# Optimization experiments

Hardware: AMD Instinct MI355X
Metric: run time of the kernel (lower is better)

## Reference

```python
import jax, jax.numpy as jnp
import numpy as np

B, S, E, H = 2, 2048, 1024, 16
D = E // H  # head dim = 64

def setup_inputs() -> dict:
    key = jax.random.key(0)
    ks = jax.random.split(key, 7)
    mk = lambda k, shape, scale=1.0: (jax.random.normal(k, shape, dtype=jnp.float32) * scale)
    return {
        "query": mk(ks[0], (B, S, E)),
        "key": mk(ks[1], (B, S, E)),
        "value": mk(ks[2], (B, S, E)),
        "Wq": mk(ks[3], (E, E), 1.0 / np.sqrt(E)),
        "Wk": mk(ks[4], (E, E), 1.0 / np.sqrt(E)),
        "Wv": mk(ks[5], (E, E), 1.0 / np.sqrt(E)),
        "Wo": mk(ks[6], (E, E), 1.0 / np.sqrt(E)),
    }

def reference(query, key, value, Wq, Wk, Wv, Wo):
    # nn.Linear(bias=False): y = x @ W.T
    def split_heads(x):
        return x.reshape(B, -1, H, D).transpose(0, 2, 1, 3)  # [B,H,S,D]
    q = split_heads(query @ Wq.T)
    k = split_heads(key @ Wk.T)
    v = split_heads(value @ Wv.T)
    scores = jnp.einsum("bhqd,bhkd->bhqk", q, k) / jnp.sqrt(jnp.float32(D))
    attn = jax.nn.softmax(scores, axis=-1)  # dropout p=0 -> identity
    out = jnp.einsum("bhqk,bhkd->bhqd", attn, v)
    out = out.transpose(0, 2, 1, 3).reshape(B, -1, E)
    out = out @ Wo.T
    return out
```

## Files before the change

### kernel.cpp

```cpp
#include <hip/hip_runtime.h>
#include <stdint.h>

#define S_LEN 2048
#define HDIM  64
#define EMB   1024
#define NTOK  4096

typedef short bf16x8 __attribute__((ext_vector_type(8)));
typedef float f32x4  __attribute__((ext_vector_type(4)));
typedef uint32_t u32x4 __attribute__((ext_vector_type(4)));
typedef uint32_t u32x2 __attribute__((ext_vector_type(2)));

__device__ __forceinline__ unsigned short f32_bf16(float f) {
  union { float f; uint32_t u; } v; v.f = f;
  return (unsigned short)((v.u + 0x7fffu + ((v.u >> 16) & 1u)) >> 16);
}

__device__ __forceinline__ uint32_t fbits(float f) {
  union { float f; uint32_t u; } v; v.f = f; return v.u;
}

__device__ __forceinline__ uint32_t pack_bf16_trunc(float lo, float hi) {
  return __builtin_amdgcn_perm(fbits(hi), fbits(lo), 0x07060302u);
}

__device__ __forceinline__ uint32_t pack_bf16_rne(float lo, float hi) {
  return (uint32_t)f32_bf16(lo) | ((uint32_t)f32_bf16(hi) << 16);
}

__device__ __forceinline__ void async_ld16(const unsigned short* g, unsigned short* l) {
  __builtin_amdgcn_global_load_lds(
      (__attribute__((address_space(1))) unsigned int*)(uintptr_t)g,
      (__attribute__((address_space(3))) unsigned int*)l, 16, 0, 0);
}

__device__ __forceinline__ void p_swap(uint32_t& x, uint32_t& y) {
  u32x2 r1 = __builtin_amdgcn_permlane32_swap(x, y, false, false);
  uint32_t a = r1[0], b = r1[1];
#if __has_builtin(__builtin_amdgcn_permlane16_swap)
  u32x2 r2 = __builtin_amdgcn_permlane16_swap(a, b, false, false);
  x = r2[0]; y = r2[1];
#else
  asm volatile("v_permlane16_swap_b32 %0, %1" : "+v"(a), "+v"(b));
  x = a; y = b;
#endif
}

__device__ __forceinline__ void block_sync_lgkm() {
  asm volatile("s_waitcnt lgkmcnt(0)" ::: "memory");
  __builtin_amdgcn_s_barrier();
}

#define CL2 0.18033688f

__global__ void cast_all(const float* __restrict__ q, const float* __restrict__ k,
                         const float* __restrict__ v, const float* __restrict__ Wq,
                         const float* __restrict__ Wk, const float* __restrict__ Wv,
                         const float* __restrict__ Wo,
                         unsigned short* __restrict__ qb, unsigned short* __restrict__ kb,
                         unsigned short* __restrict__ vb, unsigned short* __restrict__ wqb,
                         unsigned short* __restrict__ wkb, unsigned short* __restrict__ wvb,
                         unsigned short* __restrict__ wob) {
  const int b = blockIdx.x;
  const float* src; unsigned short* dst; int base;
  float scl = 1.0f;
  if (b < 12288) {
    const int which = b >> 12; base = b & 4095;
    src = which == 0 ? q : which == 1 ? k : v;
    dst = which == 0 ? qb : which == 1 ? kb : vb;
  } else {
    const int bb = b - 12288, which = bb >> 10; base = bb & 1023;
    src = which == 0 ? Wq : which == 1 ? Wk : which == 2 ? Wv : Wo;
    dst = which == 0 ? wqb : which == 1 ? wkb : which == 2 ? wvb : wob;
    if (which == 0) scl = CL2;
  }
  const int i = base * 256 + threadIdx.x;
  float4 f = ((const float4*)src)[i];
  ushort4 o;
  o.x = f32_bf16(f.x * scl); o.y = f32_bf16(f.y * scl);
  o.z = f32_bf16(f.z * scl); o.w = f32_bf16(f.w * scl);
  ((ushort4*)dst)[i] = o;
}

__global__ __launch_bounds__(256)
void gemm_qkv(const unsigned short* __restrict__ qb, const unsigned short* __restrict__ kb,
              const unsigned short* __restrict__ vb, const unsigned short* __restrict__ wqb,
              const unsigned short* __restrict__ wkb, const unsigned short* __restrict__ wvb,
              unsigned short* __restrict__ Qh, unsigned short* __restrict__ Kh,
              unsigned short* __restrict__ Vt) {
  __shared__ __align__(16) unsigned short As[2 * 128 * 32];
  __shared__ __align__(16) unsigned short Bs[2 * 128 * 32];

  const int z  = blockIdx.z;
  const int bx = blockIdx.y;
  const int by = blockIdx.x;
  const unsigned short* Xp = z == 0 ? qb  : z == 1 ? kb  : vb;
  const unsigned short* Wp = z == 0 ? wqb : z == 1 ? wkb : wvb;

  const unsigned short *A, *B;
  int tileM, tileN;
  if (z < 2) { A = Wp; tileM = bx * 128; B = Xp; tileN = by * 128; }
  else       { A = Xp; tileM = by * 128; B = Wp; tileN = bx * 128; }

  const int tid  = threadIdx.x;
  const int lane = tid & 63;
  const int wave = tid >> 6;
  const int wm = (wave >> 1) * 64;
  const int wn = (wave & 1) * 64;
  const int ccol = lane & 15;
  const int cgrp = lane >> 4;
  const int rchunk = lane >> 2;
  const int coff   = (lane & 3) * 8;

  f32x4 acc[4][4];
#pragma unroll
  for (int i = 0; i < 4; ++i)
#pragma unroll
    for (int j = 0; j < 4; ++j) acc[i][j] = 0.f;

  for (int k0 = 0; k0 < EMB; k0 += 64) {
#pragma unroll
    for (int kk = 0; kk < 2; ++kk)
#pragma unroll
      for (int i = 0; i < 2; ++i) {
        const int c = wave * 2 + i;
        const int row = c * 16 + rchunk;
        async_ld16(A + (size_t)(tileM + row) * EMB + k0 + kk * 32 + coff,
                   As + kk * 4096 + c * 512);
        async_ld16(B + (size_t)(tileN + row) * EMB + k0 + kk * 32 + coff,
                   Bs + kk * 4096 + c * 512);
      }
    __syncthreads();
#pragma unroll
    for (int kk = 0; kk < 2; ++kk) {
      bf16x8 af[4], bfm[4];
#pragma unroll
      for (int i = 0; i < 4; ++i) {
        af[i]  = *(const bf16x8*)(As + kk * 4096 + (wm + i * 16 + ccol) * 32 + cgrp * 8);
        bfm[i] = *(const bf16x8*)(Bs + kk * 4096 + (wn + i * 16 + ccol) * 32 + cgrp * 8);
      }
#pragma unroll
      for (int i = 0; i < 4; ++i)
#pragma unroll
        for (int j = 0; j < 4; ++j)
          acc[i][j] = __builtin_amdgcn_mfma_f32_16x16x32_bf16(af[i], bfm[j], acc[i][j], 0, 0, 0);
    }
    __syncthreads();
  }

  if (z < 2) {
    unsigned short* Oh = (z == 0) ? Qh : Kh;
#pragma unroll
    for (int i = 0; i < 4; ++i) {
      const int gd = tileM + wm + i * 16 + cgrp * 4;
      const int h = gd >> 6, dd = gd & 63;
#pragma unroll
      for (int j = 0; j < 4; ++j) {
        const int gt = tileN + wn + j * 16 + ccol;
        const int b = gt >> 11, s = gt & 2047;
        const uint32_t u0 = pack_bf16_rne(acc[i][j][0], acc[i][j][1]);
        const uint32_t u1 = pack_bf16_rne(acc[i][j][2], acc[i][j][3]);
        *(int2*)&Oh[((size_t)((b * 16 + h) * 2048 + s)) * 64 + dd] =
            make_int2((int)u0, (int)u1);
      }
    }
  } else {
#pragma unroll
    for (int i = 0; i < 4; ++i) {
      const int gt = tileM + wm + i * 16 + cgrp * 4;
      const int b = gt >> 11, s = gt & 2047;
#pragma unroll
      for (int j = 0; j < 4; ++j) {
        const int gd = tileN + wn + j * 16 + ccol;
        const int h = gd >> 6, dd = gd & 63;
        const uint32_t u0 = pack_bf16_rne(acc[i][j][0], acc[i][j][1]);
        const uint32_t u1 = pack_bf16_rne(acc[i][j][2], acc[i][j][3]);
        *(int2*)&Vt[((size_t)((b * 16 + h) * 64 + dd)) * 2048 + s] =
            make_int2((int)u0, (int)u1);
      }
    }
  }
}

__global__ __launch_bounds__(256)
void gemm_out(const unsigned short* __restrict__ Ctx, const unsigned short* __restrict__ Wo,
              float* __restrict__ Out) {
  __shared__ __align__(16) unsigned short As[2 * 64 * 32];
  __shared__ __align__(16) unsigned short Bs[2 * 128 * 32];

  const int tid  = threadIdx.x;
  const int lane = tid & 63;
  const int wave = tid >> 6;
  const int wm = (wave >> 1) * 32;
  const int wn = (wave & 1) * 64;
  const int ccol = lane & 15;
  const int cgrp = lane >> 4;
  const int rchunk = lane >> 2;
  const int coff   = (lane & 3) * 8;
  const int tileM = blockIdx.y * 64;
  const int tileN = blockIdx.x * 128;

  f32x4 acc[2][4];
#pragma unroll
  for (int i = 0; i < 2; ++i)
#pragma unroll
    for (int j = 0; j < 4; ++j) acc[i][j] = 0.f;

  for (int k0 = 0; k0 < EMB; k0 += 64) {
#pragma unroll
    for (int kk = 0; kk < 2; ++kk) {
      {
        const int row = wave * 16 + rchunk;
        async_ld16(Wo + (size_t)(tileM + row) * EMB + k0 + kk * 32 + coff,
                   As + kk * 2048 + wave * 512);
      }
#pragma unroll
      for (int i = 0; i < 2; ++i) {
        const int c = wave * 2 + i;
        const int row = c * 16 + rchunk;
        async_ld16(Ctx + (size_t)(tileN + row) * EMB + k0 + kk * 32 + coff,
                   Bs + kk * 4096 + c * 512);
      }
    }
    __syncthreads();
#pragma unroll
    for (int kk = 0; kk < 2; ++kk) {
      bf16x8 af[2], bfm[4];
#pragma unroll
      for (int i = 0; i < 2; ++i)
        af[i] = *(const bf16x8*)(As + kk * 2048 + (wm + i * 16 + ccol) * 32 + cgrp * 8);
#pragma unroll
      for (int j = 0; j < 4; ++j)
        bfm[j] = *(const bf16x8*)(Bs + kk * 4096 + (wn + j * 16 + ccol) * 32 + cgrp * 8);
#pragma unroll
      for (int i = 0; i < 2; ++i)
#pragma unroll
        for (int j = 0; j < 4; ++j)
          acc[i][j] = __builtin_amdgcn_mfma_f32_16x16x32_bf16(af[i], bfm[j], acc[i][j], 0, 0, 0);
    }
    __syncthreads();
  }

#pragma unroll
  for (int i = 0; i < 2; ++i) {
    const int odim = tileM + wm + i * 16 + cgrp * 4;
#pragma unroll
    for (int j = 0; j < 4; ++j) {
      const int gt = tileN + wn + j * 16 + ccol;
      float4 o = make_float4(acc[i][j][0], acc[i][j][1], acc[i][j][2], acc[i][j][3]);
      *(float4*)&Out[(size_t)gt * 1024 + odim] = o;
    }
  }
}

__global__ __launch_bounds__(256, 2)
void attn_kernel(const unsigned short* __restrict__ Qh,
                 const unsigned short* __restrict__ Kh,
                 const unsigned short* __restrict__ Vt,
                 unsigned short* __restrict__ Ctx) {
  __shared__ __align__(16) unsigned short Ks[2 * 64 * 64];
  __shared__ __align__(16) unsigned short Vs[3 * 64 * 64];
  __shared__ __align__(16) unsigned short Ps[128 * 64];

  const int tid  = threadIdx.x;
  const int lane = tid & 63;
  const int wave = tid >> 6;
  const int bh = blockIdx.x;
  const int q0 = blockIdx.y * 128;
  const unsigned short* Qg = Qh + ((size_t)bh * S_LEN + q0) * HDIM;
  const unsigned short* Kg = Kh + (size_t)bh * S_LEN * HDIM;
  const unsigned short* Vg = Vt + (size_t)bh * HDIM * S_LEN;

  const int ccol = lane & 15;
  const int cgrp = lane >> 4;
  const int mrow = wave * 32;
  const int sw7  = ccol & 7;

#pragma unroll
  for (int i = 0; i < 4; ++i) {
    const int cid = i * 256 + tid;
    const int row = cid >> 3, j = cid & 7, g = j ^ (row & 7);
    *(int4*)&Ps[row * 64 + j * 8] = *(const int4*)&Qg[(size_t)row * 64 + g * 8];
  }

  const int r0 = tid >> 3, j0 = tid & 7;
  const int r1 = r0 + 32;
  const int sA = j0 ^ (r0 & 7);
  const int sB = j0 ^ (r1 & 7);

  int4 kr0 = *(const int4*)&Kg[(size_t)r0 * 64 + sA * 8];
  int4 kr1 = *(const int4*)&Kg[(size_t)r1 * 64 + sB * 8];
  int4 vr0 = *(const int4*)&Vg[(size_t)r0 * 2048 + sA * 8];
  int4 vr1 = *(const int4*)&Vg[(size_t)r1 * 2048 + sB * 8];

  __syncthreads();

  bf16x8 aq[2][2];
#pragma unroll
  for (int g = 0; g < 2; ++g)
#pragma unroll
    for (int kk = 0; kk < 2; ++kk) {
      const int pp = (kk * 4 + cgrp) ^ sw7;
      aq[g][kk] = *(const bf16x8*)&Ps[(mrow + g * 16 + ccol) * 64 + pp * 8];
    }

  *(int4*)&Ks[r0 * 64 + j0 * 8] = kr0;
  *(int4*)&Ks[r1 * 64 + j0 * 8] = kr1;
  *(int4*)&Vs[r0 * 64 + j0 * 8] = vr0;
  *(int4*)&Vs[r1 * 64 + j0 * 8] = vr1;
  kr0 = *(const int4*)&Kg[(size_t)(64 + r0) * 64 + sA * 8];
  kr1 = *(const int4*)&Kg[(size_t)(64 + r1) * 64 + sB * 8];
  vr0 = *(const int4*)&Vg[(size_t)r0 * 2048 + 64 + sA * 8];
  vr1 = *(const int4*)&Vg[(size_t)r1 * 2048 + 64 + sB * 8];
  block_sync_lgkm();

  f32x4 l4[2];
  l4[0] = 0.f; l4[1] = 0.f;
  f32x4 o_acc[4][2];
#pragma unroll
  for (int dt = 0; dt < 4; ++dt) { o_acc[dt][0] = 0.f; o_acc[dt][1] = 0.f; }

  bf16x8 ap[2][2];

  for (int i = 0; i < 32; ++i) {
    unsigned short* Kb = Ks + (i & 1) * 4096;

    __builtin_amdgcn_s_setprio(1);
    f32x4 sc[2][4];
#pragma unroll
    for (int nt = 0; nt < 4; ++nt) {
      const int krow = nt * 16 + ccol;
      bf16x8 ak0 = *(const bf16x8*)&Kb[krow * 64 + ((cgrp) ^ sw7) * 8];
      bf16x8 ak1 = *(const bf16x8*)&Kb[krow * 64 + ((4 + cgrp) ^ sw7) * 8];
#pragma unroll
      for (int g = 0; g < 2; ++g) {
        f32x4 s = 0.f;
        s = __builtin_amdgcn_mfma_f32_16x16x32_bf16(ak0, aq[g][0], s, 0, 0, 0);
        s = __builtin_amdgcn_mfma_f32_16x16x32_bf16(ak1, aq[g][1], s, 0, 0, 0);
        sc[g][nt] = s;
      }
    }

    if (i > 0) {
      unsigned short* Vp = Vs + ((i - 1) % 3) * 4096;
#pragma unroll
      for (int dt = 0; dt < 4; ++dt) {
        const int vrow = dt * 16 + ccol;
        bf16x8 av0 = *(const bf16x8*)&Vp[vrow * 64 + ((cgrp) ^ sw7) * 8];
        bf16x8 av1 = *(const bf16x8*)&Vp[vrow * 64 + ((4 + cgrp) ^ sw7) * 8];
#pragma unroll
        for (int g = 0; g < 2; ++g) {
          f32x4 o = o_acc[dt][g];
          o = __builtin_amdgcn_mfma_f32_16x16x32_bf16(av0, ap[g][0], o, 0, 0, 0);
          o = __builtin_amdgcn_mfma_f32_16x16x32_bf16(av1, ap[g][1], o, 0, 0, 0);
          o_acc[dt][g] = o;
        }
      }
    }
    __builtin_amdgcn_s_setprio(0);

    if (i < 31) {
      unsigned short* Kn = Ks + ((i + 1) & 1) * 4096;
      unsigned short* Vn = Vs + ((i + 1) % 3) * 4096;
      *(int4*)&Kn[r0 * 64 + j0 * 8] = kr0;
      *(int4*)&Kn[r1 * 64 + j0 * 8] = kr1;
      *(int4*)&Vn[r0 * 64 + j0 * 8] = vr0;
      *(int4*)&Vn[r1 * 64 + j0 * 8] = vr1;
      if (i < 30) {
        const int nb = (i + 2) * 64;
        kr0 = *(const int4*)&Kg[(size_t)(nb + r0) * 64 + sA * 8];
        kr1 = *(const int4*)&Kg[(size_t)(nb + r1) * 64 + sB * 8];
        vr0 = *(const int4*)&Vg[(size_t)r0 * 2048 + nb + sA * 8];
        vr1 = *(const int4*)&Vg[(size_t)r1 * 2048 + nb + sB * 8];
      }
    }

#pragma unroll
    for (int g = 0; g < 2; ++g)
#pragma unroll
      for (int nt = 0; nt < 4; ++nt) {
#pragma unroll
        for (int r = 0; r < 4; ++r)
          sc[g][nt][r] = __builtin_amdgcn_exp2f(sc[g][nt][r]);
        l4[g] += sc[g][nt];
      }

#pragma unroll
    for (int g = 0; g < 2; ++g) {
      uint32_t u[4][2];
#pragma unroll
      for (int nt = 0; nt < 4; ++nt) {
        u[nt][0] = pack_bf16_trunc(sc[g][nt][0], sc[g][nt][1]);
        u[nt][1] = pack_bf16_trunc(sc[g][nt][2], sc[g][nt][3]);
      }
      uint32_t w[2][4];
#pragma unroll
      for (int kk = 0; kk < 2; ++kk)
#pragma unroll
        for (int h = 0; h < 2; ++h) {
          uint32_t x = u[2 * kk][h], y = u[2 * kk + 1][h];
          p_swap(x, y);
          w[kk][h] = x; w[kk][2 + h] = y;
        }
#pragma unroll
      for (int kk = 0; kk < 2; ++kk) {
        union { u32x4 u; bf16x8 b; } cv;
        cv.u[0] = w[kk][0]; cv.u[1] = w[kk][1];
        cv.u[2] = w[kk][2]; cv.u[3] = w[kk][3];
        ap[g][kk] = cv.b;
      }
    }

    block_sync_lgkm();
  }

  {
    unsigned short* Vp = Vs + (31 % 3) * 4096;
    __builtin_amdgcn_s_setprio(1);
#pragma unroll
    for (int dt = 0; dt < 4; ++dt) {
      const int vrow = dt * 16 + ccol;
      bf16x8 av0 = *(const bf16x8*)&Vp[vrow * 64 + ((cgrp) ^ sw7) * 8];
      bf16x8 av1 = *(const bf16x8*)&Vp[vrow * 64 + ((4 + cgrp) ^ sw7) * 8];
#pragma unroll
      for (int g = 0; g < 2; ++g) {
        f32x4 o = o_acc[dt][g];
        o = __builtin_amdgcn_mfma_f32_16x16x32_bf16(av0, ap[g][0], o, 0, 0, 0);
        o = __builtin_amdgcn_mfma_f32_16x16x32_bf16(av1, ap[g][1], o, 0, 0, 0);
        o_acc[dt][g] = o;
      }
    }
    __builtin_amdgcn_s_setprio(0);
  }

  const int b = bh >> 4, h = bh & 15;
#pragma unroll
  for (int g = 0; g < 2; ++g) {
    float l_i = l4[g][0] + l4[g][1] + l4[g][2] + l4[g][3];
    l_i += __shfl_xor(l_i, 16);
    l_i += __shfl_xor(l_i, 32);
    const float inv_l = __builtin_amdgcn_rcpf(l_i) * 1.00195f;
    const int srow = q0 + mrow + g * 16 + ccol;
#pragma unroll
    for (int dt = 0; dt < 4; ++dt) {
      float o0 = o_acc[dt][g][0] * inv_l, o1 = o_acc[dt][g][1] * inv_l;
      float o2 = o_acc[dt][g][2] * inv_l, o3 = o_acc[dt][g][3] * inv_l;
      uint32_t u0 = pack_bf16_rne(o0, o1);
      uint32_t u1 = pack_bf16_rne(o2, o3);
      const int col = h * 64 + dt * 16 + cgrp * 4;
      *(int2*)&Ctx[((size_t)(b * 2048 + srow)) * 1024 + col] = make_int2((int)u0, (int)u1);
    }
  }
}

extern "C" void kernel_launch(void* const* d_in, const int* in_sizes, int n_in,
                              void* d_out, int out_size, void* d_ws, size_t ws_size,
                              hipStream_t stream) {
  const float* q  = (const float*)d_in[0];
  const float* k  = (const float*)d_in[1];
  const float* v  = (const float*)d_in[2];
  const float* Wq = (const float*)d_in[3];
  const float* Wk = (const float*)d_in[4];
  const float* Wv = (const float*)d_in[5];
  const float* Wo = (const float*)d_in[6];

  const size_t tok = (size_t)NTOK * EMB;
  const size_t wsz = (size_t)EMB * EMB;
  unsigned short* p = (unsigned short*)d_ws;
  unsigned short* qb  = p; p += tok;
  unsigned short* kb  = p; p += tok;
  unsigned short* vb  = p; p += tok;
  unsigned short* wqb = p; p += wsz;
  unsigned short* wkb = p; p += wsz;
  unsigned short* wvb = p; p += wsz;
  unsigned short* wob = p; p += wsz;
  unsigned short* Qh  = p; p += tok;
  unsigned short* Kh  = p; p += tok;
  unsigned short* Vt  = p; p += tok;
  unsigned short* Ctx = p; p += tok;

  cast_all<<<dim3(16384), dim3(256), 0, stream>>>(q, k, v, Wq, Wk, Wv, Wo,
                                                  qb, kb, vb, wqb, wkb, wvb, wob);

  gemm_qkv<<<dim3(32, 8, 3), dim3(256), 0, stream>>>(qb, kb, vb, wqb, wkb, wvb,
                                                     Qh, Kh, Vt);

  attn_kernel<<<dim3(32, 16), dim3(256), 0, stream>>>(Qh, Kh, Vt, Ctx);

  gemm_out<<<dim3(32, 16), dim3(256), 0, stream>>>(Ctx, wob, (float*)d_out);
}
```

Measured before the change: 212.8 us.

## Process two KV tiles per barrier with four-stage LDS ring and deeper prefetch

The attention loop now handles two 64-key tiles per iteration with a single block barrier, using a 4-slot LDS ring for K and V and two register prefetch sets loaded two tiles ahead. The PV product is done in the same tile rather than software-pipelined one tile behind. The aim is to halve the barrier count and deepen global prefetch to hide latency. In exchange it uses more LDS (which may lower occupancy), holds more prefetch registers, and removes the QK/PV overlap across tiles.

```diff
diff --git a/kernel.cpp b/kernel.cpp
--- a/kernel.cpp
+++ b/kernel.cpp
@@ -258,8 +258,8 @@
                  const unsigned short* __restrict__ Kh,
                  const unsigned short* __restrict__ Vt,
                  unsigned short* __restrict__ Ctx) {
-  __shared__ __align__(16) unsigned short Ks[2 * 64 * 64];
-  __shared__ __align__(16) unsigned short Vs[3 * 64 * 64];
+  __shared__ __align__(16) unsigned short Ks[4 * 64 * 64];
+  __shared__ __align__(16) unsigned short Vs[4 * 64 * 64];
   __shared__ __align__(16) unsigned short Ps[128 * 64];
 
   const int tid  = threadIdx.x;
@@ -288,10 +288,14 @@
   const int sA = j0 ^ (r0 & 7);
   const int sB = j0 ^ (r1 & 7);
 
-  int4 kr0 = *(const int4*)&Kg[(size_t)r0 * 64 + sA * 8];
-  int4 kr1 = *(const int4*)&Kg[(size_t)r1 * 64 + sB * 8];
-  int4 vr0 = *(const int4*)&Vg[(size_t)r0 * 2048 + sA * 8];
-  int4 vr1 = *(const int4*)&Vg[(size_t)r1 * 2048 + sB * 8];
+  int4 ka0 = *(const int4*)&Kg[(size_t)r0 * 64 + sA * 8];
+  int4 ka1 = *(const int4*)&Kg[(size_t)r1 * 64 + sB * 8];
+  int4 va0 = *(const int4*)&Vg[(size_t)r0 * 2048 + sA * 8];
+  int4 va1 = *(const int4*)&Vg[(size_t)r1 * 2048 + sB * 8];
+  int4 kb0 = *(const int4*)&Kg[(size_t)(64 + r0) * 64 + sA * 8];
+  int4 kb1 = *(const int4*)&Kg[(size_t)(64 + r1) * 64 + sB * 8];
+  int4 vb0 = *(const int4*)&Vg[(size_t)r0 * 2048 + 64 + sA * 8];
+  int4 vb1 = *(const int4*)&Vg[(size_t)r1 * 2048 + 64 + sB * 8];
 
   __syncthreads();
 
@@ -304,14 +308,22 @@
       aq[g][kk] = *(const bf16x8*)&Ps[(mrow + g * 16 + ccol) * 64 + pp * 8];
     }
 
-  *(int4*)&Ks[r0 * 64 + j0 * 8] = kr0;
-  *(int4*)&Ks[r1 * 64 + j0 * 8] = kr1;
-  *(int4*)&Vs[r0 * 64 + j0 * 8] = vr0;
-  *(int4*)&Vs[r1 * 64 + j0 * 8] = vr1;
-  kr0 = *(const int4*)&Kg[(size_t)(64 + r0) * 64 + sA * 8];
-  kr1 = *(const int4*)&Kg[(size_t)(64 + r1) * 64 + sB * 8];
-  vr0 = *(const int4*)&Vg[(size_t)r0 * 2048 + 64 + sA * 8];
-  vr1 = *(const int4*)&Vg[(size_t)r1 * 2048 + 64 + sB * 8];
+  *(int4*)&Ks[r0 * 64 + j0 * 8] = ka0;
+  *(int4*)&Ks[r1 * 64 + j0 * 8] = ka1;
+  *(int4*)&Vs[r0 * 64 + j0 * 8] = va0;
+  *(int4*)&Vs[r1 * 64 + j0 * 8] = va1;
+  *(int4*)&Ks[4096 + r0 * 64 + j0 * 8] = kb0;
+  *(int4*)&Ks[4096 + r1 * 64 + j0 * 8] = kb1;
+  *(int4*)&Vs[4096 + r0 * 64 + j0 * 8] = vb0;
+  *(int4*)&Vs[4096 + r1 * 64 + j0 * 8] = vb1;
+  ka0 = *(const int4*)&Kg[(size_t)(128 + r0) * 64 + sA * 8];
+  ka1 = *(const int4*)&Kg[(size_t)(128 + r1) * 64 + sB * 8];
+  va0 = *(const int4*)&Vg[(size_t)r0 * 2048 + 128 + sA * 8];
+  va1 = *(const int4*)&Vg[(size_t)r1 * 2048 + 128 + sB * 8];
+  kb0 = *(const int4*)&Kg[(size_t)(192 + r0) * 64 + sA * 8];
+  kb1 = *(const int4*)&Kg[(size_t)(192 + r1) * 64 + sB * 8];
+  vb0 = *(const int4*)&Vg[(size_t)r0 * 2048 + 192 + sA * 8];
+  vb1 = *(const int4*)&Vg[(size_t)r1 * 2048 + 192 + sB * 8];
   block_sync_lgkm();
 
   f32x4 l4[2];
@@ -320,34 +332,88 @@
 #pragma unroll
   for (int dt = 0; dt < 4; ++dt) { o_acc[dt][0] = 0.f; o_acc[dt][1] = 0.f; }
 
-  bf16x8 ap[2][2];
-
-  for (int i = 0; i < 32; ++i) {
-    unsigned short* Kb = Ks + (i & 1) * 4096;
-
-    __builtin_amdgcn_s_setprio(1);
-    f32x4 sc[2][4];
-#pragma unroll
-    for (int nt = 0; nt < 4; ++nt) {
-      const int krow = nt * 16 + ccol;
-      bf16x8 ak0 = *(const bf16x8*)&Kb[krow * 64 + ((cgrp) ^ sw7) * 8];
-      bf16x8 ak1 = *(const bf16x8*)&Kb[krow * 64 + ((4 + cgrp) ^ sw7) * 8];
+  for (int j = 0; j < 16; ++j) {
+    {
+      const int t0 = 2 * j;
+      const unsigned short* Kb = Ks + (t0 & 3) * 4096;
+      const unsigned short* Vb = Vs + (t0 & 3) * 4096;
+
+      f32x4 sc[2][4];
+      __builtin_amdgcn_s_setprio(1);
+#pragma unroll
+      for (int nt = 0; nt < 4; ++nt) {
+        const int krow = nt * 16 + ccol;
+        bf16x8 ak0 = *(const bf16x8*)&Kb[krow * 64 + ((cgrp) ^ sw7) * 8];
+        bf16x8 ak1 = *(const bf16x8*)&Kb[krow * 64 + ((4 + cgrp) ^ sw7) * 8];
+#pragma unroll
+        for (int g = 0; g < 2; ++g) {
+          f32x4 s = 0.f;
+          s = __builtin_amdgcn_mfma_f32_16x16x32_bf16(ak0, aq[g][0], s, 0, 0, 0);
+          s = __builtin_amdgcn_mfma_f32_16x16x32_bf16(ak1, aq[g][1], s, 0, 0, 0);
+          sc[g][nt] = s;
+        }
+      }
+      __builtin_amdgcn_s_setprio(0);
+
+      if (j < 15) {
+        unsigned short* Kn = Ks + ((t0 + 2) & 3) * 4096;
+        unsigned short* Vn = Vs + ((t0 + 2) & 3) * 4096;
+        *(int4*)&Kn[r0 * 64 + j0 * 8] = ka0;
+        *(int4*)&Kn[r1 * 64 + j0 * 8] = ka1;
+        *(int4*)&Vn[r0 * 64 + j0 * 8] = va0;
+        *(int4*)&Vn[r1 * 64 + j0 * 8] = va1;
+        if (j < 14) {
+          const int nb = (t0 + 4) * 64;
+          ka0 = *(const int4*)&Kg[(size_t)(nb + r0) * 64 + sA * 8];
+          ka1 = *(const int4*)&Kg[(size_t)(nb + r1) * 64 + sB * 8];
+          va0 = *(const int4*)&Vg[(size_t)r0 * 2048 + nb + sA * 8];
+          va1 = *(const int4*)&Vg[(size_t)r1 * 2048 + nb + sB * 8];
+        }
+      }
+
+#pragma unroll
+      for (int g = 0; g < 2; ++g)
+#pragma unroll
+        for (int nt = 0; nt < 4; ++nt) {
+#pragma unroll
+          for (int r = 0; r < 4; ++r)
+            sc[g][nt][r] = __builtin_amdgcn_exp2f(sc[g][nt][r]);
+          l4[g] += sc[g][nt];
+        }
+
+      bf16x8 ap[2][2];
 #pragma unroll
       for (int g = 0; g < 2; ++g) {
-        f32x4 s = 0.f;
-        s = __builtin_amdgcn_mfma_f32_16x16x32_bf16(ak0, aq[g][0], s, 0, 0, 0);
-        s = __builtin_amdgcn_mfma_f32_16x16x32_bf16(ak1, aq[g][1], s, 0, 0, 0);
-        sc[g][nt] = s;
-      }
-    }
-
-    if (i > 0) {
-      unsigned short* Vp = Vs + ((i - 1) % 3) * 4096;
+        uint32_t u[4][2];
+#pragma unroll
+        for (int nt = 0; nt < 4; ++nt) {
+          u[nt][0] = pack_bf16_trunc(sc[g][nt][0], sc[g][nt][1]);
+          u[nt][1] = pack_bf16_trunc(sc[g][nt][2], sc[g][nt][3]);
+        }
+        uint32_t w[2][4];
+#pragma unroll
+        for (int kk = 0; kk < 2; ++kk)
+#pragma unroll
+          for (int h = 0; h < 2; ++h) {
+            uint32_t x = u[2 * kk][h], y = u[2 * kk + 1][h];
+            p_swap(x, y);
+            w[kk][h] = x; w[kk][2 + h] = y;
+          }
+#pragma unroll
+        for (int kk = 0; kk < 2; ++kk) {
+          union { u32x4 u; bf16x8 b; } cv;
+          cv.u[0] = w[kk][0]; cv.u[1] = w[kk][1];
+          cv.u[2] = w[kk][2]; cv.u[3] = w[kk][3];
+          ap[g][kk] = cv.b;
+        }
+      }
+
+      __builtin_amdgcn_s_setprio(1);
 #pragma unroll
       for (int dt = 0; dt < 4; ++dt) {
         const int vrow = dt * 16 + ccol;
-        bf16x8 av0 = *(const bf16x8*)&Vp[vrow * 64 + ((cgrp) ^ sw7) * 8];
-        bf16x8 av1 = *(const bf16x8*)&Vp[vrow * 64 + ((4 + cgrp) ^ sw7) * 8];
+        bf16x8 av0 = *(const bf16x8*)&Vb[vrow * 64 + ((cgrp) ^ sw7) * 8];
+        bf16x8 av1 = *(const bf16x8*)&Vb[vrow * 64 + ((4 + cgrp) ^ sw7) * 8];
 #pragma unroll
         for (int g = 0; g < 2; ++g) {
           f32x4 o = o_acc[dt][g];
@@ -356,81 +422,102 @@
           o_acc[dt][g] = o;
         }
       }
-    }
-    __builtin_amdgcn_s_setprio(0);
-
-    if (i < 31) {
-      unsigned short* Kn = Ks + ((i + 1) & 1) * 4096;
-      unsigned short* Vn = Vs + ((i + 1) % 3) * 4096;
-      *(int4*)&Kn[r0 * 64 + j0 * 8] = kr0;
-      *(int4*)&Kn[r1 * 64 + j0 * 8] = kr1;
-      *(int4*)&Vn[r0 * 64 + j0 * 8] = vr0;
-      *(int4*)&Vn[r1 * 64 + j0 * 8] = vr1;
-      if (i < 30) {
-        const int nb = (i + 2) * 64;
-        kr0 = *(const int4*)&Kg[(size_t)(nb + r0) * 64 + sA * 8];
-        kr1 = *(const int4*)&Kg[(size_t)(nb + r1) * 64 + sB * 8];
-        vr0 = *(const int4*)&Vg[(size_t)r0 * 2048 + nb + sA * 8];
-        vr1 = *(const int4*)&Vg[(size_t)r1 * 2048 + nb + sB * 8];
-      }
-    }
-
-#pragma unroll
-    for (int g = 0; g < 2; ++g)
+      __builtin_amdgcn_s_setprio(0);
+    }
+
+    {
+      const int t1 = 2 * j + 1;
+      const unsigned short* Kb = Ks + (t1 & 3) * 4096;
+      const unsigned short* Vb = Vs + (t1 & 3) * 4096;
+
+      f32x4 sc[2][4];
+      __builtin_amdgcn_s_setprio(1);
 #pragma unroll
       for (int nt = 0; nt < 4; ++nt) {
-#pragma unroll
-        for (int r = 0; r < 4; ++r)
-          sc[g][nt][r] = __builtin_amdgcn_exp2f(sc[g][nt][r]);
-        l4[g] += sc[g][nt];
-      }
-
-#pragma unroll
-    for (int g = 0; g < 2; ++g) {
-      uint32_t u[4][2];
-#pragma unroll
-      for (int nt = 0; nt < 4; ++nt) {
-        u[nt][0] = pack_bf16_trunc(sc[g][nt][0], sc[g][nt][1]);
-        u[nt][1] = pack_bf16_trunc(sc[g][nt][2], sc[g][nt][3]);
-      }
-      uint32_t w[2][4];
-#pragma unroll
-      for (int kk = 0; kk < 2; ++kk)
-#pragma unroll
-        for (int h = 0; h < 2; ++h) {
-          uint32_t x = u[2 * kk][h], y = u[2 * kk + 1][h];
-          p_swap(x, y);
-          w[kk][h] = x; w[kk][2 + h] = y;
-        }
-#pragma unroll
-      for (int kk = 0; kk < 2; ++kk) {
-        union { u32x4 u; bf16x8 b; } cv;
-        cv.u[0] = w[kk][0]; cv.u[1] = w[kk][1];
-        cv.u[2] = w[kk][2]; cv.u[3] = w[kk][3];
-        ap[g][kk] = cv.b;
-      }
+        const int krow = nt * 16 + ccol;
+        bf16x8 ak0 = *(const bf16x8*)&Kb[krow * 64 + ((cgrp) ^ sw7) * 8];
+        bf16x8 ak1 = *(const bf16x8*)&Kb[krow * 64 + ((4 + cgrp) ^ sw7) * 8];
+#pragma unroll
+        for (int g = 0; g < 2; ++g) {
+          f32x4 s = 0.f;
+          s = __builtin_amdgcn_mfma_f32_16x16x32_bf16(ak0, aq[g][0], s, 0, 0, 0);
+          s = __builtin_amdgcn_mfma_f32_16x16x32_bf16(ak1, aq[g][1], s, 0, 0, 0);
+          sc[g][nt] = s;
+        }
+      }
+      __builtin_amdgcn_s_setprio(0);
+
+      if (j < 15) {
+        unsigned short* Kn = Ks + ((t1 + 2) & 3) * 4096;
+        unsigned short* Vn = Vs + ((t1 + 2) & 3) * 4096;
+        *(int4*)&Kn[r0 * 64 + j0 * 8] = kb0;
+        *(int4*)&Kn[r1 * 64 + j0 * 8] = kb1;
+        *(int4*)&Vn[r0 * 64 + j0 * 8] = vb0;
+        *(int4*)&Vn[r1 * 64 + j0 * 8] = vb1;
+        if (j < 14) {
+          const int nb = (t1 + 4) * 64;
+          kb0 = *(const int4*)&Kg[(size_t)(nb + r0) * 64 + sA * 8];
+          kb1 = *(const int4*)&Kg[(size_t)(nb + r1) * 64 + sB * 8];
+          vb0 = *(const int4*)&Vg[(size_t)r0 * 2048 + nb + sA * 8];
+          vb1 = *(const int4*)&Vg[(size_t)r1 * 2048 + nb + sB * 8];
+        }
+      }
+
+#pragma unroll
+      for (int g = 0; g < 2; ++g)
+#pragma unroll
+        for (int nt = 0; nt < 4; ++nt) {
+#pragma unroll
+          for (int r = 0; r < 4; ++r)
+            sc[g][nt][r] = __builtin_amdgcn_exp2f(sc[g][nt][r]);
+          l4[g] += sc[g][nt];
+        }
+
+      bf16x8 ap[2][2];
+#pragma unroll
+      for (int g = 0; g < 2; ++g) {
+        uint32_t u[4][2];
+#pragma unroll
+        for (int nt = 0; nt < 4; ++nt) {
+          u[nt][0] = pack_bf16_trunc(sc[g][nt][0], sc[g][nt][1]);
+          u[nt][1] = pack_bf16_trunc(sc[g][nt][2], sc[g][nt][3]);
+        }
+        uint32_t w[2][4];
+#pragma unroll
+        for (int kk = 0; kk < 2; ++kk)
+#pragma unroll
+          for (int h = 0; h < 2; ++h) {
+            uint32_t x = u[2 * kk][h], y = u[2 * kk + 1][h];
+            p_swap(x, y);
+            w[kk][h] = x; w[kk][2 + h] = y;
+          }
+#pragma unroll
+        for (int kk = 0; kk < 2; ++kk) {
+          union { u32x4 u; bf16x8 b; } cv;
+          cv.u[0] = w[kk][0]; cv.u[1] = w[kk][1];
+          cv.u[2] = w[kk][2]; cv.u[3] = w[kk][3];
+          ap[g][kk] = cv.b;
+        }
+      }
+
+      __builtin_amdgcn_s_setprio(1);
+#pragma unroll
+      for (int dt = 0; dt < 4; ++dt) {
+        const int vrow = dt * 16 + ccol;
+        bf16x8 av0 = *(const bf16x8*)&Vb[vrow * 64 + ((cgrp) ^ sw7) * 8];
+        bf16x8 av1 = *(const bf16x8*)&Vb[vrow * 64 + ((4 + cgrp) ^ sw7) * 8];
+#pragma unroll
+        for (int g = 0; g < 2; ++g) {
+          f32x4 o = o_acc[dt][g];
+          o = __builtin_amdgcn_mfma_f32_16x16x32_bf16(av0, ap[g][0], o, 0, 0, 0);
+          o = __builtin_amdgcn_mfma_f32_16x16x32_bf16(av1, ap[g][1], o, 0, 0, 0);
+          o_acc[dt][g] = o;
+        }
+      }
+      __builtin_amdgcn_s_setprio(0);
     }
 
     block_sync_lgkm();
-  }
-
-  {
-    unsigned short* Vp = Vs + (31 % 3) * 4096;
-    __builtin_amdgcn_s_setprio(1);
-#pragma unroll
-    for (int dt = 0; dt < 4; ++dt) {
-      const int vrow = dt * 16 + ccol;
-      bf16x8 av0 = *(const bf16x8*)&Vp[vrow * 64 + ((cgrp) ^ sw7) * 8];
-      bf16x8 av1 = *(const bf16x8*)&Vp[vrow * 64 + ((4 + cgrp) ^ sw7) * 8];
-#pragma unroll
-      for (int g = 0; g < 2; ++g) {
-        f32x4 o = o_acc[dt][g];
-        o = __builtin_amdgcn_mfma_f32_16x16x32_bf16(av0, ap[g][0], o, 0, 0, 0);
-        o = __builtin_amdgcn_mfma_f32_16x16x32_bf16(av1, ap[g][1], o, 0, 0, 0);
-        o_acc[dt][g] = o;
-      }
-    }
-    __builtin_amdgcn_s_setprio(0);
   }
 
   const int b = bh >> 4, h = bh & 15;
```

After: 206.3 us (median of 2 runs). -3.1%, faster.
